# Kernel tuning notes

Measured on AMD Instinct MI355X. Metric: run time of the kernel, lower is better.

The kernel has to match this reference:

```python
import jax, jax.numpy as jnp
import numpy as np

B, T, D = 1, 2048, 2048
N_HEADS, N_KV = 32, 8
HD = D // N_HEADS          # 64
G = N_HEADS // N_KV        # 4 query heads per kv head


def setup_inputs() -> dict:
    key = jax.random.key(0)
    ks = jax.random.split(key, 8)
    x = jax.random.normal(ks[0], (B, T, D), dtype=jnp.float32)
    cos = jax.random.uniform(ks[1], (1, 1, T, HD), dtype=jnp.float32)
    sin = jax.random.uniform(ks[2], (1, 1, T, HD), dtype=jnp.float32)
    attention_mask = jnp.ones((B, T), dtype=jnp.int32)
    s = 1.0 / np.sqrt(D)
    Wq = jax.random.normal(ks[3], (D, D), dtype=jnp.float32) * s
    Wk = jax.random.normal(ks[4], (D, N_KV * HD), dtype=jnp.float32) * s
    Wv = jax.random.normal(ks[5], (D, N_KV * HD), dtype=jnp.float32) * s
    Wo = jax.random.normal(ks[6], (D, D), dtype=jnp.float32) * s
    return {"x": x, "cos": cos, "sin": sin, "attention_mask": attention_mask,
            "Wq": Wq, "Wk": Wk, "Wv": Wv, "Wo": Wo}


def rotate_half(t):
    t1, t2 = jnp.split(t, 2, axis=-1)
    return jnp.concatenate((-t2, t1), axis=-1)


def reference(x, cos, sin, attention_mask, Wq, Wk, Wv, Wo):
    b, t, d = x.shape
    # projections (Linear, no bias); weights stored as [in, out]
    q = (x @ Wq).reshape(b, t, N_HEADS, HD).transpose(0, 2, 1, 3)   # [B,H,T,hd]
    k = (x @ Wk).reshape(b, t, N_KV, HD).transpose(0, 2, 1, 3)      # [B,Kv,T,hd]
    v = (x @ Wv).reshape(b, t, N_KV, HD).transpose(0, 2, 1, 3)      # [B,Kv,T,hd]
    # RoPE
    q = q * cos + rotate_half(q) * sin
    k = k * cos + rotate_half(k) * sin
    # GQA without materializing repeated KV: group query heads by kv head
    qg = q.reshape(b, N_KV, G, t, HD)                               # [B,Kv,G,T,hd]
    scale = 1.0 / jnp.sqrt(jnp.asarray(HD, dtype=x.dtype))
    scores = jnp.einsum('bkgqd,bkcd->bkgqc', qg, k) * scale          # [B,Kv,G,T,T]
    neg = jnp.finfo(x.dtype).min
    # padding mask: (1 - mask) * finfo.min, broadcast over heads/query pos
    pad = (1.0 - attention_mask.astype(x.dtype)) * neg               # [B,T]
    scores = scores + pad[:, None, None, None, :]
    # causal mask
    causal = jnp.tril(jnp.ones((t, t), dtype=bool))
    scores = jnp.where(causal[None, None, None, :, :], scores, neg)
    p = jax.nn.softmax(scores, axis=-1)
    y = jnp.einsum('bkgqc,bkcd->bkgqd', p, v)                        # [B,Kv,G,T,hd]
    y = y.reshape(b, N_HEADS, t, HD).transpose(0, 2, 1, 3).reshape(b, t, d)
    return y @ Wo
```

## Files before the change

kernel.cpp:

```cpp
#include <hip/hip_runtime.h>
#include <hip/hip_bf16.h>
#include <math.h>

typedef __attribute__((ext_vector_type(4))) float f32x4;
typedef __attribute__((ext_vector_type(8))) short bf16x8;
typedef __attribute__((ext_vector_type(4))) short bf16x4;
typedef unsigned short u16;
typedef unsigned int u32;


__device__ __forceinline__ float exp2fast(float x) {
    return __builtin_amdgcn_exp2f(x);
}
__device__ __forceinline__ u16 f2bf(float f) {
    return __builtin_bit_cast(u16, __float2bfloat16(f));
}
__device__ __forceinline__ float bf2f(u16 h) {
    return __builtin_bit_cast(float, ((u32)h) << 16);
}

#define GLL16(gsrc, ldst) __builtin_amdgcn_global_load_lds( \
    (const __attribute__((address_space(1))) u32*)(gsrc),   \
    (__attribute__((address_space(3))) u32*)(ldst), 16, 0, 0)

__device__ __forceinline__ void tconv64(const float* __restrict__ in, u16* __restrict__ out,
                                        int R, int C, int bx, int by,
                                        float (*tile)[65], int tx, int ty) {
    int c0 = bx * 64, r0 = by * 64;
    #pragma unroll
    for (int i = 0; i < 16; ++i)
        tile[ty + i * 4][tx] = in[(size_t)(r0 + ty + i * 4) * C + c0 + tx];
    __syncthreads();
    #pragma unroll
    for (int i = 0; i < 16; ++i)
        out[(size_t)(c0 + ty + i * 4) * R + r0 + tx] = f2bf(tile[tx][ty + i * 4]);
}

__global__ void k_prep(const float* __restrict__ x, u16* __restrict__ xb,
                       const float* __restrict__ Wq, const float* __restrict__ Wk,
                       const float* __restrict__ Wv, const float* __restrict__ Wo,
                       u16* __restrict__ Wt, u16* __restrict__ WoT,
                       const int* __restrict__ maskp, float* __restrict__ padf,
                       int* __restrict__ padAny) {
    __shared__ float tile[64][65];
    const int r = blockIdx.x;
    const int tx = threadIdx.x, ty = threadIdx.y;
    const int tid = ty * 64 + tx;
    if (r < 4096) {
        int base = (r * 256 + tid) * 4;
        float4 v = *(const float4*)(x + base);
        ushort4 o;
        o.x = f2bf(v.x); o.y = f2bf(v.y); o.z = f2bf(v.z); o.w = f2bf(v.w);
        *(ushort4*)(xb + base) = o;
    } else if (r < 5120) {
        int rr = r - 4096;  tconv64(Wq, Wt, 2048, 2048, rr & 31, rr >> 5, tile, tx, ty);
    } else if (r < 5376) {
        int rr = r - 5120;  tconv64(Wk, Wt + (size_t)2048 * 2048, 2048, 512, rr & 7, rr >> 3, tile, tx, ty);
    } else if (r < 5632) {
        int rr = r - 5376;  tconv64(Wv, Wt + (size_t)2560 * 2048, 2048, 512, rr & 7, rr >> 3, tile, tx, ty);
    } else if (r < 6656) {
        int rr = r - 5632;  tconv64(Wo, WoT, 2048, 2048, rr & 31, rr >> 5, tile, tx, ty);
    } else if (r < 6664) {
        int t = (r - 6656) * 256 + tid;
        padf[t] = maskp[t] ? 0.0f : -3.4028235e38f;
    } else {
        if (tid < 32) {
            int any = 0;
            for (int i = 0; i < 64; ++i) any |= (maskp[tid * 64 + i] == 0);
            padAny[tid] = any;
        }
    }
}

__global__ void k_vprep(const u16* __restrict__ QKV, u16* __restrict__ Vt) {
    __shared__ u16 tile[32][34];
    const int r = blockIdx.x;
    const int tx = threadIdx.x, ty = threadIdx.y;
    int c0 = (r & 15) * 32, r0 = (r >> 4) * 32;
    const u16* in = QKV + 2560;
    #pragma unroll
    for (int i = 0; i < 4; ++i)
        tile[ty + i * 8][tx] = in[(size_t)(r0 + ty + i * 8) * 3072 + c0 + tx];
    __syncthreads();
    int kv = r0 + tx;
    int kvp = (kv & ~63) + (((kv >> 5) & 1) << 5) + (((kv >> 2) & 3) << 3)
            + (((kv >> 4) & 1) << 2) + (kv & 3);
    #pragma unroll
    for (int i = 0; i < 4; ++i)
        Vt[(size_t)(c0 + ty + i * 8) * 2048 + kvp] = tile[tx][ty + i * 8];
}

template<int OUTF32, int ROPE>
__global__ __launch_bounds__(256) void k_gemm(const u16* __restrict__ A, int lda,
                                              const u16* __restrict__ Bt,
                                              void* __restrict__ Cv,
                                              int M, int N, int K,
                                              const float* __restrict__ cosp,
                                              const float* __restrict__ sinp) {
    __shared__ u16 As[2][64 * 64];
    __shared__ u16 Bs[2][128 * 64];
    const int tid = threadIdx.x;
    const int w = tid >> 6, lane = tid & 63;
    const int wr = w & 1, wc = w >> 1;
    const int g = lane >> 4, l15 = lane & 15;
    const int m0 = blockIdx.y * 64, n0 = blockIdx.x * 128;

    f32x4 acc[2][4] = {};

    const u16* gA[2];
    const u16* gB[4];
    #pragma unroll
    for (int i = 0; i < 2; ++i) {
        int c = tid + i * 256;
        int rr = c >> 3, kc = (c & 7) ^ (rr & 7);
        gA[i] = A + (size_t)(m0 + rr) * lda + kc * 8;
    }
    #pragma unroll
    for (int i = 0; i < 4; ++i) {
        int c = tid + i * 256;
        int rr = c >> 3, kc = (c & 7) ^ (rr & 7);
        gB[i] = Bt + (size_t)(n0 + rr) * K + kc * 8;
    }

    auto stageAB = [&](int b, int k0) {
        #pragma unroll
        for (int i = 0; i < 2; ++i)
            GLL16(gA[i] + k0, &As[b][(tid + i * 256) * 8]);
        #pragma unroll
        for (int i = 0; i < 4; ++i)
            GLL16(gB[i] + k0, &Bs[b][(tid + i * 256) * 8]);
    };

    stageAB(0, 0);
    __syncthreads();
    int buf = 0;

    for (int k0 = 0; k0 < K; k0 += 64) {
        int kn = k0 + 64;
        if (kn < K) stageAB(buf ^ 1, kn);

        bf16x8 af[2][2], bfr[4][2];
        #pragma unroll
        for (int mt = 0; mt < 2; ++mt) {
            int row = wr * 32 + mt * 16 + l15;
            int rb = row * 64;
            #pragma unroll
            for (int kk = 0; kk < 2; ++kk) {
                int slot = (kk * 4 + g) ^ (row & 7);
                af[mt][kk] = *(const bf16x8*)&As[buf][rb + slot * 8];
            }
        }
        #pragma unroll
        for (int nt = 0; nt < 4; ++nt) {
            int row = wc * 64 + nt * 16 + l15;
            int rb = row * 64;
            #pragma unroll
            for (int kk = 0; kk < 2; ++kk) {
                int slot = (kk * 4 + g) ^ (row & 7);
                bfr[nt][kk] = *(const bf16x8*)&Bs[buf][rb + slot * 8];
            }
        }
        #pragma unroll
        for (int mt = 0; mt < 2; ++mt)
            #pragma unroll
            for (int nt = 0; nt < 4; ++nt) {
                acc[mt][nt] = __builtin_amdgcn_mfma_f32_16x16x32_bf16(af[mt][0], bfr[nt][0], acc[mt][nt], 0, 0, 0);
                acc[mt][nt] = __builtin_amdgcn_mfma_f32_16x16x32_bf16(af[mt][1], bfr[nt][1], acc[mt][nt], 0, 0, 0);
            }
        __syncthreads();
        buf ^= 1;
    }

    if (ROPE && n0 < 2560) {
        const float sc = (n0 < 2048) ? 0.18033688f : 1.0f;
        #pragma unroll
        for (int mt = 0; mt < 2; ++mt) {
            #pragma unroll
            for (int rr = 0; rr < 4; ++rr) {
                int t = m0 + wr * 32 + mt * 16 + g * 4 + rr;
                #pragma unroll
                for (int nt = 0; nt < 2; ++nt) {
                    int jh = nt * 16 + l15;
                    float c1 = cosp[t * 64 + jh],      s1 = sinp[t * 64 + jh];
                    float c2 = cosp[t * 64 + jh + 32], s2 = sinp[t * 64 + jh + 32];
                    float a = acc[mt][nt][rr], b = acc[mt][nt + 2][rr];
                    acc[mt][nt][rr]     = (a * c1 - b * s1) * sc;
                    acc[mt][nt + 2][rr] = (b * c2 + a * s2) * sc;
                }
            }
        }
    }

    #pragma unroll
    for (int mt = 0; mt < 2; ++mt) {
        #pragma unroll
        for (int nt = 0; nt < 4; ++nt) {
            int mrow = m0 + wr * 32 + mt * 16 + g * 4;
            int ncol = n0 + wc * 64 + nt * 16 + l15;
            #pragma unroll
            for (int rr = 0; rr < 4; ++rr) {
                float v = acc[mt][nt][rr];
                if (OUTF32) ((float*)Cv)[(size_t)(mrow + rr) * N + ncol] = v;
                else        ((u16*)Cv)[(size_t)(mrow + rr) * N + ncol] = f2bf(v);
            }
        }
    }
}

__global__ __launch_bounds__(512) void k_attn(const u16* __restrict__ QKV,
                                              const u16* __restrict__ VtG,
                                              const float* __restrict__ padf,
                                              const int* __restrict__ padAny,
                                              u16* __restrict__ Ob) {
    __shared__ u16 Ks[2][64 * 64];
    __shared__ u16 Vs[2][64 * 64];
    const int kvh = blockIdx.y;
    const int x = (int)blockIdx.x;
    const int tid = threadIdx.x;
    const int w = tid >> 6, lane = tid & 63;
    const int g = lane >> 4, l15 = lane & 15;
    const int h = kvh * 4 + (w & 3);
    int qA, qB;
    if (kvh < 4) { qA = x;      qB = 127 - x; }
    else         { qA = 63 - x; qB = 64 + x;  }
    const int q0w = ((w >> 2) == 0 ? qA : qB) * 16;
    const int q = q0w + l15;
    const int myfull = q0w >> 6;
    const int iters = ((qB * 16) >> 6) + 1;
    const bf16x8 ones8 = {(short)0x3F80, (short)0x3F80, (short)0x3F80, (short)0x3F80,
                          (short)0x3F80, (short)0x3F80, (short)0x3F80, (short)0x3F80};

    const u16* qrow = QKV + (size_t)q * 3072 + h * 64;
    bf16x8 qf0 = *(const bf16x8*)(qrow + g * 8);
    bf16x8 qf1 = *(const bf16x8*)(qrow + 32 + g * 8);

    f32x4 oacc[4] = {};
    float l_run = 0.0f;

    auto stage = [&](int b, int kv0) {
        int p = tid;
        int rr = p >> 3, c = p & 7;
        int cs = c ^ (rr & 7);
        GLL16(QKV + (size_t)(kv0 + rr) * 3072 + 2048 + kvh * 64 + cs * 8, &Ks[b][p * 8]);
        GLL16(VtG + (size_t)(kvh * 64 + rr) * 2048 + kv0 + cs * 8, &Vs[b][p * 8]);
    };

    stage(0, 0);
    __syncthreads();
    int buf = 0;

    for (int t = 0; t < iters; ++t) {
        const int kv0 = t * 64;
        if (t + 1 < iters) stage(buf ^ 1, kv0 + 64);

        if (t <= myfull) {
            const bool masked = (t == myfull);

            f32x4 st[4];
            __builtin_amdgcn_s_setprio(1);
            #pragma unroll
            for (int j = 0; j < 4; ++j) {
                int row = j * 16 + l15;
                int rb = row * 64, sw = (row & 7) << 3;
                bf16x8 kf0 = *(const bf16x8*)&Ks[buf][rb + ((g << 3) ^ sw)];
                bf16x8 kf1 = *(const bf16x8*)&Ks[buf][rb + ((32 + (g << 3)) ^ sw)];
                f32x4 z = {};
                st[j] = __builtin_amdgcn_mfma_f32_16x16x32_bf16(kf0, qf0, z, 0, 0, 0);
                st[j] = __builtin_amdgcn_mfma_f32_16x16x32_bf16(kf1, qf1, st[j], 0, 0, 0);
            }
            __builtin_amdgcn_s_setprio(0);

            if (padAny[t]) {
                #pragma unroll
                for (int j = 0; j < 4; ++j) {
                    f32x4 pd = *(const f32x4*)(padf + kv0 + j * 16 + g * 4);
                    #pragma unroll
                    for (int rr = 0; rr < 4; ++rr) st[j][rr] += pd[rr];
                }
            }
            if (masked) {
                #pragma unroll
                for (int j = 0; j < 4; ++j)
                    #pragma unroll
                    for (int rr = 0; rr < 4; ++rr) {
                        int kv = kv0 + j * 16 + g * 4 + rr;
                        if (kv > q) st[j][rr] = -INFINITY;
                    }
            }
            bf16x4 pb[4];
            #pragma unroll
            for (int j = 0; j < 4; ++j)
                #pragma unroll
                for (int rr = 0; rr < 4; ++rr)
                    pb[j][rr] = (short)f2bf(exp2fast(st[j][rr]));
            bf16x8 pbp0 = {pb[0][0], pb[0][1], pb[0][2], pb[0][3],
                           pb[1][0], pb[1][1], pb[1][2], pb[1][3]};
            bf16x8 pbp1 = {pb[2][0], pb[2][1], pb[2][2], pb[2][3],
                           pb[3][0], pb[3][1], pb[3][2], pb[3][3]};

            __builtin_amdgcn_s_setprio(1);
            {
                f32x4 la = {};
                la = __builtin_amdgcn_mfma_f32_16x16x32_bf16(ones8, pbp0, la, 0, 0, 0);
                la = __builtin_amdgcn_mfma_f32_16x16x32_bf16(ones8, pbp1, la, 0, 0, 0);
                l_run += la[0];
            }
            #pragma unroll
            for (int dt = 0; dt < 4; ++dt) {
                int row = dt * 16 + l15;
                int rb = row * 64, sw7 = row & 7;
                bf16x8 v0 = *(const bf16x8*)&Vs[buf][rb + ((g ^ sw7) << 3)];
                bf16x8 v1 = *(const bf16x8*)&Vs[buf][rb + (((4 + g) ^ sw7) << 3)];
                oacc[dt] = __builtin_amdgcn_mfma_f32_16x16x32_bf16(v0, pbp0, oacc[dt], 0, 0, 0);
                oacc[dt] = __builtin_amdgcn_mfma_f32_16x16x32_bf16(v1, pbp1, oacc[dt], 0, 0, 0);
            }
            __builtin_amdgcn_s_setprio(0);
        }
        __syncthreads();
        buf ^= 1;
    }

    float il = 1.0f / l_run;
    u16* orow = Ob + (size_t)q * 3072 + h * 64;
    #pragma unroll
    for (int dt = 0; dt < 4; ++dt) {
        ushort4 o;
        o.x = f2bf(oacc[dt][0] * il);
        o.y = f2bf(oacc[dt][1] * il);
        o.z = f2bf(oacc[dt][2] * il);
        o.w = f2bf(oacc[dt][3] * il);
        *(ushort4*)(orow + dt * 16 + g * 4) = o;
    }
}

extern "C" void kernel_launch(void* const* d_in, const int* in_sizes, int n_in,
                              void* d_out, int out_size, void* d_ws, size_t ws_size,
                              hipStream_t stream) {
    const float* x    = (const float*)d_in[0];
    const float* cosp = (const float*)d_in[1];
    const float* sinp = (const float*)d_in[2];
    const int*   mask = (const int*)d_in[3];
    const float* Wq   = (const float*)d_in[4];
    const float* Wk   = (const float*)d_in[5];
    const float* Wv   = (const float*)d_in[6];
    const float* Wo   = (const float*)d_in[7];
    float* out = (float*)d_out;

    char* ws = (char*)d_ws;
    u16* xb  = (u16*)ws; ws += (size_t)2048 * 2048 * 2;
    u16* Wt  = (u16*)ws; ws += (size_t)3072 * 2048 * 2;
    u16* WoT = (u16*)ws; ws += (size_t)2048 * 2048 * 2;
    u16* QKV = (u16*)ws; ws += (size_t)2048 * 3072 * 2;
    u16* Vt  = (u16*)ws; ws += (size_t)512 * 2048 * 2;
    float* padf = (float*)ws; ws += 2048 * 4;
    int* padAny = (int*)ws;

    k_prep<<<6665, dim3(64, 4), 0, stream>>>(x, xb, Wq, Wk, Wv, Wo, Wt, WoT, mask, padf, padAny);

    k_gemm<0, 1><<<dim3(24, 32), 256, 0, stream>>>(xb, 2048, Wt, QKV, 2048, 3072, 2048, cosp, sinp);

    k_vprep<<<1024, dim3(32, 8), 0, stream>>>(QKV, Vt);

    k_attn<<<dim3(64, 8), 512, 0, stream>>>(QKV, Vt, padf, padAny, QKV);

    k_gemm<1, 0><<<dim3(16, 32), 256, 0, stream>>>(QKV, 3072, WoT, out, 2048, 2048, 2048, nullptr, nullptr);
}
```

Before: 121.0 us.

## Double KV tile to 128 rows in attention with per-tile causal subtile skipping

The attention kernel now stages 128 keys/values per iteration instead of 64, which halves the number of loop iterations and __syncthreads barriers. On the diagonal tile it computes only the 16-row key subtiles up to the wave's query block (jm), skipping fully masked work. LDS use doubles to 64KB per block, which may lower occupancy, and the runtime-bounded subtile guards may add branching or register pressure.

```diff
diff --git a/kernel.cpp b/kernel.cpp
--- a/kernel.cpp
+++ b/kernel.cpp
@@ -212,8 +212,8 @@
                                               const float* __restrict__ padf,
                                               const int* __restrict__ padAny,
                                               u16* __restrict__ Ob) {
-    __shared__ u16 Ks[2][64 * 64];
-    __shared__ u16 Vs[2][64 * 64];
+    __shared__ u16 Ks[2][128 * 64];
+    __shared__ u16 Vs[2][128 * 64];
     const int kvh = blockIdx.y;
     const int x = (int)blockIdx.x;
     const int tid = threadIdx.x;
@@ -225,8 +225,9 @@
     else         { qA = 63 - x; qB = 64 + x;  }
     const int q0w = ((w >> 2) == 0 ? qA : qB) * 16;
     const int q = q0w + l15;
-    const int myfull = q0w >> 6;
-    const int iters = ((qB * 16) >> 6) + 1;
+    const int myfull = q0w >> 7;
+    const int jmd = ((q0w & 127) >> 4) + 1;
+    const int iters = ((qB * 16) >> 7) + 1;
     const bf16x8 ones8 = {(short)0x3F80, (short)0x3F80, (short)0x3F80, (short)0x3F80,
                           (short)0x3F80, (short)0x3F80, (short)0x3F80, (short)0x3F80};
 
@@ -238,11 +239,16 @@
     float l_run = 0.0f;
 
     auto stage = [&](int b, int kv0) {
-        int p = tid;
-        int rr = p >> 3, c = p & 7;
-        int cs = c ^ (rr & 7);
-        GLL16(QKV + (size_t)(kv0 + rr) * 3072 + 2048 + kvh * 64 + cs * 8, &Ks[b][p * 8]);
-        GLL16(VtG + (size_t)(kvh * 64 + rr) * 2048 + kv0 + cs * 8, &Vs[b][p * 8]);
+        #pragma unroll
+        for (int i = 0; i < 2; ++i) {
+            int p = tid + i * 512;
+            int rk = p >> 3;
+            int ck = (p & 7) ^ (rk & 7);
+            GLL16(QKV + (size_t)(kv0 + rk) * 3072 + 2048 + kvh * 64 + ck * 8, &Ks[b][p * 8]);
+            int rv = (p & 511) >> 3;
+            int cv = (p & 7) ^ (rv & 7);
+            GLL16(VtG + (size_t)(kvh * 64 + rv) * 2048 + kv0 + i * 64 + cv * 8, &Vs[b][p * 8]);
+        }
     };
 
     stage(0, 0);
@@ -250,16 +256,17 @@
     int buf = 0;
 
     for (int t = 0; t < iters; ++t) {
-        const int kv0 = t * 64;
-        if (t + 1 < iters) stage(buf ^ 1, kv0 + 64);
+        const int kv0 = t * 128;
+        if (t + 1 < iters) stage(buf ^ 1, kv0 + 128);
 
         if (t <= myfull) {
             const bool masked = (t == myfull);
-
-            f32x4 st[4];
+            const int jm = masked ? jmd : 8;
+
+            f32x4 st[8];
             __builtin_amdgcn_s_setprio(1);
             #pragma unroll
-            for (int j = 0; j < 4; ++j) {
+            for (int j = 0; j < 8; ++j) if (j < jm) {
                 int row = j * 16 + l15;
                 int rb = row * 64, sw = (row & 7) << 3;
                 bf16x8 kf0 = *(const bf16x8*)&Ks[buf][rb + ((g << 3) ^ sw)];
@@ -270,9 +277,9 @@
             }
             __builtin_amdgcn_s_setprio(0);
 
-            if (padAny[t]) {
-                #pragma unroll
-                for (int j = 0; j < 4; ++j) {
+            if (padAny[2 * t] | padAny[2 * t + 1]) {
+                #pragma unroll
+                for (int j = 0; j < 8; ++j) if (j < jm) {
                     f32x4 pd = *(const f32x4*)(padf + kv0 + j * 16 + g * 4);
                     #pragma unroll
                     for (int rr = 0; rr < 4; ++rr) st[j][rr] += pd[rr];
@@ -280,39 +287,46 @@
             }
             if (masked) {
                 #pragma unroll
-                for (int j = 0; j < 4; ++j)
+                for (int j = 0; j < 8; ++j) if (j < jm) {
                     #pragma unroll
                     for (int rr = 0; rr < 4; ++rr) {
                         int kv = kv0 + j * 16 + g * 4 + rr;
                         if (kv > q) st[j][rr] = -INFINITY;
                     }
-            }
-            bf16x4 pb[4];
-            #pragma unroll
-            for (int j = 0; j < 4; ++j)
+                }
+            }
+            bf16x4 pb[8] = {};
+            #pragma unroll
+            for (int j = 0; j < 8; ++j) if (j < jm) {
                 #pragma unroll
                 for (int rr = 0; rr < 4; ++rr)
                     pb[j][rr] = (short)f2bf(exp2fast(st[j][rr]));
-            bf16x8 pbp0 = {pb[0][0], pb[0][1], pb[0][2], pb[0][3],
-                           pb[1][0], pb[1][1], pb[1][2], pb[1][3]};
-            bf16x8 pbp1 = {pb[2][0], pb[2][1], pb[2][2], pb[2][3],
-                           pb[3][0], pb[3][1], pb[3][2], pb[3][3]};
+            }
+            bf16x8 pbp[4];
+            #pragma unroll
+            for (int pr = 0; pr < 4; ++pr)
+                pbp[pr] = bf16x8{pb[2 * pr][0], pb[2 * pr][1], pb[2 * pr][2], pb[2 * pr][3],
+                                 pb[2 * pr + 1][0], pb[2 * pr + 1][1], pb[2 * pr + 1][2], pb[2 * pr + 1][3]};
 
             __builtin_amdgcn_s_setprio(1);
             {
                 f32x4 la = {};
-                la = __builtin_amdgcn_mfma_f32_16x16x32_bf16(ones8, pbp0, la, 0, 0, 0);
-                la = __builtin_amdgcn_mfma_f32_16x16x32_bf16(ones8, pbp1, la, 0, 0, 0);
+                #pragma unroll
+                for (int pr = 0; pr < 4; ++pr) if (2 * pr < jm)
+                    la = __builtin_amdgcn_mfma_f32_16x16x32_bf16(ones8, pbp[pr], la, 0, 0, 0);
                 l_run += la[0];
             }
             #pragma unroll
             for (int dt = 0; dt < 4; ++dt) {
                 int row = dt * 16 + l15;
                 int rb = row * 64, sw7 = row & 7;
-                bf16x8 v0 = *(const bf16x8*)&Vs[buf][rb + ((g ^ sw7) << 3)];
-                bf16x8 v1 = *(const bf16x8*)&Vs[buf][rb + (((4 + g) ^ sw7) << 3)];
-                oacc[dt] = __builtin_amdgcn_mfma_f32_16x16x32_bf16(v0, pbp0, oacc[dt], 0, 0, 0);
-                oacc[dt] = __builtin_amdgcn_mfma_f32_16x16x32_bf16(v1, pbp1, oacc[dt], 0, 0, 0);
+                #pragma unroll
+                for (int pr = 0; pr < 4; ++pr) if (2 * pr < jm) {
+                    int vblk = pr >> 1;
+                    int sl = (pr & 1) ? (4 + g) : g;
+                    bf16x8 v = *(const bf16x8*)&Vs[buf][vblk * 4096 + rb + ((sl ^ sw7) << 3)];
+                    oacc[dt] = __builtin_amdgcn_mfma_f32_16x16x32_bf16(v, pbp[pr], oacc[dt], 0, 0, 0);
+                }
             }
             __builtin_amdgcn_s_setprio(0);
         }
```

Measured after the change: 123.6 us. +2.1%, slower.
